# Optimization experiments

Hardware: AMD Instinct MI355X
Metric: run time of the kernel (lower is better)

## Reference

```python
import jax, jax.numpy as jnp
import numpy as np

B = 64      # batch
T = 32      # frames per clip
H = 256     # hidden_dim
NMAX = 64   # max boxes per batch element


def _n_per_frame():
    rng = np.random.default_rng(0)
    return rng.integers(32, NMAX + 1, size=B)  # each n <= NMAX


def setup_inputs() -> dict:
    n = _n_per_frame()
    N = int(n.sum())  # total boxes across batch (~3072)
    key = jax.random.key(0)
    k1, k2, k3 = jax.random.split(key, 3)
    bbox = jax.random.uniform(k1, (N * T, 4), dtype=jnp.float32)
    W1 = jax.random.normal(k2, (4, 128), dtype=jnp.float32) * 0.5
    b1 = jnp.zeros((128,), jnp.float32)
    W2 = jax.random.normal(k3, (128, H), dtype=jnp.float32) * 0.0884  # ~1/sqrt(128)
    b2 = jnp.zeros((H,), jnp.float32)
    return {
        "bbox": bbox,
        "W1": W1, "b1": b1, "W2": W2, "b2": b2,
        "n_per_frame": jnp.asarray(n, jnp.int32),
        "n_max": NMAX,
    }


def reference(bbox, W1, b1, W2, b2, n_per_frame, n_max):
    N = bbox.shape[0] // T  # static total box count
    # tiny MLP: 4 -> 128 -> H
    pos = (jax.nn.relu(bbox @ W1 + b1) @ W2 + b2).reshape(N, T, H)
    # ragged scatter into padded (B*n_max, T, H) tensor
    frame_id = jnp.repeat(jnp.arange(B), n_per_frame, total_repeat_length=N)  # [N]
    starts = jnp.cumsum(n_per_frame) - n_per_frame                            # exclusive cumsum [B]
    local = jnp.arange(N) - starts[frame_id]                                  # slot within frame
    tgt = frame_id * n_max + local                                            # [N] unique targets
    pos_pad = jnp.zeros((B * n_max, T, H), pos.dtype).at[tgt].set(pos)
    # (B, n_max, T, H) -> (B, T, n_max, H) -> (B*T, n_max, H) -> (n_max, B*T, H)
    out = (pos_pad.reshape(B, n_max, T, H)
           .transpose(0, 2, 1, 3)
           .reshape(B * T, n_max, H)
           .transpose(1, 0, 2))
    return out
```

## Files before the change

kernel.cpp:

```cpp
#include <hip/hip_runtime.h>

#define B_ 64
#define T_ 32
#define H_ 256
#define NMAX_ 64
#define TILES 2048
#define GRID 512
#define BLOCK 256

typedef __attribute__((ext_vector_type(8))) short short8;
typedef __attribute__((ext_vector_type(4))) float f32x4;

__device__ __forceinline__ short f2bf(float f) {
    unsigned u = __builtin_bit_cast(unsigned, f);
    u = (u + 0x7fffu + ((u >> 16) & 1u)) >> 16;
    return (short)u;
}

__global__ __launch_bounds__(BLOCK, 2)
void pe_fused(const float* __restrict__ bbox,
              const float* __restrict__ W1,
              const float* __restrict__ b1,
              const float* __restrict__ W2,
              const float* __restrict__ b2,
              const int*   __restrict__ npf,
              float* __restrict__ out,
              int NT)
{
    __shared__ float W1s[512];
    __shared__ float b1s[128];
    __shared__ int   s_n[64];
    __shared__ int   s_start[64];
    __shared__ short Hs[2][64 * 136];

    const int tid  = threadIdx.x;
    const int wave = tid >> 6;
    const int lane = tid & 63;
    const int q    = lane >> 4;
    const int m16  = lane & 15;

    if (tid < 256) { W1s[tid] = W1[tid]; W1s[tid + 256] = W1[tid + 256]; }
    if (tid < 128) b1s[tid] = b1[tid];

    if (wave == 0) {
        int v = npf[lane];
        s_n[lane] = v;
        int s = v;
#pragma unroll
        for (int d = 1; d < 64; d <<= 1) {
            int u = __shfl_up(s, d, 64);
            if (lane >= d) s += u;
        }
        s_start[lane] = s - v;
    }

    short8 Bf[4][4];
    float  b2v[4];
#pragma unroll
    for (int ct = 0; ct < 4; ++ct) {
        const int n = wave * 64 + ct * 16 + m16;
        b2v[ct] = b2[n];
#pragma unroll
        for (int kc = 0; kc < 4; ++kc) {
            const int k0 = kc * 32 + q * 8;
            short8 f;
#pragma unroll
            for (int jj = 0; jj < 8; ++jj)
                f[jj] = f2bf(W2[(k0 + jj) * H_ + n]);
            Bf[ct][kc] = f;
        }
    }
    __syncthreads();

    const int r4 = tid >> 2;
    const int c4 = tid & 3;

    int pbuf = 0;

    for (int tt = blockIdx.x; tt < TILES; tt += GRID) {
        const int b  = tt >> 5;
        const int l0 = (tt & 31) * 2;
        const int nb = s_n[b];

        const int ob0 = (l0 * (B_ * T_) + b * T_) * H_;
        const int ob1 = ob0 + (B_ * T_) * H_;

        if (l0 >= nb) {
            const float4 z = make_float4(0.f, 0.f, 0.f, 0.f);
#pragma unroll
            for (int rr = 0; rr < 16; ++rr) {
                const int r = rr * 4 + wave;
                float* dst = out + (r < 32 ? ob0 + r * H_ : ob1 + (r - 32) * H_);
                *(float4*)(dst + lane * 4) = z;
            }
            continue;
        }

        const int sb = s_start[b];

        {
            const int gr = (sb + l0) * T_ + r4;
            float4 bb = make_float4(0.f, 0.f, 0.f, 0.f);
            if (gr < NT) bb = *(const float4*)(bbox + gr * 4);
            short* hrow = &Hs[pbuf][r4 * 136 + c4 * 32];
#pragma unroll
            for (int w = 0; w < 4; ++w) {
                short8 hv;
#pragma unroll
                for (int jj = 0; jj < 8; ++jj) {
                    const int h = c4 * 32 + w * 8 + jj;
                    float v = b1s[h];
                    v = fmaf(bb.x, W1s[h],       v);
                    v = fmaf(bb.y, W1s[128 + h], v);
                    v = fmaf(bb.z, W1s[256 + h], v);
                    v = fmaf(bb.w, W1s[384 + h], v);
                    v = fmaxf(v, 0.f);
                    hv[jj] = f2bf(v);
                }
                *(short8*)(hrow + w * 8) = hv;
            }
        }
        __syncthreads();

        f32x4 acc[4][4];
#pragma unroll
        for (int rt = 0; rt < 4; ++rt)
#pragma unroll
            for (int ct = 0; ct < 4; ++ct)
                acc[rt][ct] = (f32x4){0.f, 0.f, 0.f, 0.f};

#pragma unroll
        for (int kc = 0; kc < 4; ++kc) {
            short8 a[4];
#pragma unroll
            for (int rt = 0; rt < 4; ++rt)
                a[rt] = *(const short8*)&Hs[pbuf][(rt * 16 + m16) * 136 + kc * 32 + q * 8];
#pragma unroll
            for (int rt = 0; rt < 4; ++rt)
#pragma unroll
                for (int ct = 0; ct < 4; ++ct)
                    acc[rt][ct] = __builtin_amdgcn_mfma_f32_16x16x32_bf16(
                        a[rt], Bf[ct][kc], acc[rt][ct], 0, 0, 0);
        }
        pbuf ^= 1;

        const bool v1 = (l0 + 1) < nb;
#pragma unroll
        for (int rt = 0; rt < 4; ++rt) {
#pragma unroll
            for (int reg = 0; reg < 4; ++reg) {
                const int rl = rt * 16 + q * 4 + reg;
                const bool ok = (rl < 32) | v1;
                float* dst = out + (rl < 32 ? ob0 + rl * H_ : ob1 + (rl - 32) * H_)
                                 + wave * 64 + m16;
#pragma unroll
                for (int ct = 0; ct < 4; ++ct)
                    dst[ct * 16] = ok ? (acc[rt][ct][reg] + b2v[ct]) : 0.f;
            }
        }
    }
}

extern "C" void kernel_launch(void* const* d_in, const int* in_sizes, int n_in,
                              void* d_out, int out_size, void* d_ws, size_t ws_size,
                              hipStream_t stream)
{
    const float* bbox = (const float*)d_in[0];
    const float* W1   = (const float*)d_in[1];
    const float* b1   = (const float*)d_in[2];
    const float* W2   = (const float*)d_in[3];
    const float* b2   = (const float*)d_in[4];
    const int*   npf  = (const int*)d_in[5];
    const int NT = in_sizes[0] / 4;

    pe_fused<<<GRID, BLOCK, 0, stream>>>(bbox, W1, b1, W2, b2, npf,
                                         (float*)d_out, NT);
}
```

Measured before the change: 157.2 us.

## Swap MFMA operands for float4 stores, prefetch bbox, use lighter barrier

Swaps the A/B operands of the MFMA so each lane's accumulator holds four consecutive output columns, which lets the epilogue write float4 vector stores instead of scalar stores. The bias b2 is loaded as float4 to match. All four tiles' bbox rows are prefetched into registers before the loop, and the loop is fully unrolled. __syncthreads is replaced by an inline-asm barrier that waits only on LDS counters, so outstanding global stores no longer block the barrier. This raises register pressure and relies on the fixed GRID*4 == TILES mapping.

```diff
diff --git a/kernel.cpp b/kernel.cpp
--- a/kernel.cpp
+++ b/kernel.cpp
@@ -15,6 +15,10 @@
     unsigned u = __builtin_bit_cast(unsigned, f);
     u = (u + 0x7fffu + ((u >> 16) & 1u)) >> 16;
     return (short)u;
+}
+
+__device__ __forceinline__ void barrier_nodrain() {
+    asm volatile("s_waitcnt lgkmcnt(0)\n\ts_barrier" ::: "memory");
 }
 
 __global__ __launch_bounds__(BLOCK, 2)
@@ -54,20 +58,19 @@
         s_start[lane] = s - v;
     }
 
-    short8 Bf[4][4];
-    float  b2v[4];
+    short8 Wf[4][4];
+    float4 b2q[4];
 #pragma unroll
     for (int ct = 0; ct < 4; ++ct) {
-        const int n = wave * 64 + ct * 16 + m16;
-        b2v[ct] = b2[n];
+        b2q[ct] = *(const float4*)(b2 + wave * 64 + ct * 16 + q * 4);
 #pragma unroll
         for (int kc = 0; kc < 4; ++kc) {
             const int k0 = kc * 32 + q * 8;
             short8 f;
 #pragma unroll
             for (int jj = 0; jj < 8; ++jj)
-                f[jj] = f2bf(W2[(k0 + jj) * H_ + n]);
-            Bf[ct][kc] = f;
+                f[jj] = f2bf(W2[(k0 + jj) * H_ + wave * 64 + ct * 16 + m16]);
+            Wf[ct][kc] = f;
         }
     }
     __syncthreads();
@@ -75,9 +78,22 @@
     const int r4 = tid >> 2;
     const int c4 = tid & 3;
 
+    float4 bb[4];
+#pragma unroll
+    for (int i = 0; i < 4; ++i) {
+        const int tt = blockIdx.x + i * GRID;
+        const int b  = tt >> 5;
+        const int l0 = (tt & 31) * 2;
+        const int g  = (s_start[b] + l0) * T_ + r4;
+        bb[i] = make_float4(0.f, 0.f, 0.f, 0.f);
+        if (g < NT) bb[i] = *(const float4*)(bbox + g * 4);
+    }
+
     int pbuf = 0;
 
-    for (int tt = blockIdx.x; tt < TILES; tt += GRID) {
+#pragma unroll
+    for (int i = 0; i < 4; ++i) {
+        const int tt = blockIdx.x + i * GRID;
         const int b  = tt >> 5;
         const int l0 = (tt & 31) * 2;
         const int nb = s_n[b];
@@ -96,12 +112,8 @@
             continue;
         }
 
-        const int sb = s_start[b];
-
         {
-            const int gr = (sb + l0) * T_ + r4;
-            float4 bb = make_float4(0.f, 0.f, 0.f, 0.f);
-            if (gr < NT) bb = *(const float4*)(bbox + gr * 4);
+            const float4 bv = bb[i];
             short* hrow = &Hs[pbuf][r4 * 136 + c4 * 32];
 #pragma unroll
             for (int w = 0; w < 4; ++w) {
@@ -110,52 +122,54 @@
                 for (int jj = 0; jj < 8; ++jj) {
                     const int h = c4 * 32 + w * 8 + jj;
                     float v = b1s[h];
-                    v = fmaf(bb.x, W1s[h],       v);
-                    v = fmaf(bb.y, W1s[128 + h], v);
-                    v = fmaf(bb.z, W1s[256 + h], v);
-                    v = fmaf(bb.w, W1s[384 + h], v);
+                    v = fmaf(bv.x, W1s[h],       v);
+                    v = fmaf(bv.y, W1s[128 + h], v);
+                    v = fmaf(bv.z, W1s[256 + h], v);
+                    v = fmaf(bv.w, W1s[384 + h], v);
                     v = fmaxf(v, 0.f);
                     hv[jj] = f2bf(v);
                 }
                 *(short8*)(hrow + w * 8) = hv;
             }
         }
-        __syncthreads();
+        barrier_nodrain();
 
         f32x4 acc[4][4];
 #pragma unroll
-        for (int rt = 0; rt < 4; ++rt)
+        for (int ct = 0; ct < 4; ++ct)
 #pragma unroll
-            for (int ct = 0; ct < 4; ++ct)
-                acc[rt][ct] = (f32x4){0.f, 0.f, 0.f, 0.f};
+            for (int rt = 0; rt < 4; ++rt)
+                acc[ct][rt] = (f32x4){0.f, 0.f, 0.f, 0.f};
 
 #pragma unroll
         for (int kc = 0; kc < 4; ++kc) {
-            short8 a[4];
+            short8 hf[4];
 #pragma unroll
             for (int rt = 0; rt < 4; ++rt)
-                a[rt] = *(const short8*)&Hs[pbuf][(rt * 16 + m16) * 136 + kc * 32 + q * 8];
+                hf[rt] = *(const short8*)&Hs[pbuf][(rt * 16 + m16) * 136 + kc * 32 + q * 8];
 #pragma unroll
-            for (int rt = 0; rt < 4; ++rt)
+            for (int ct = 0; ct < 4; ++ct)
 #pragma unroll
-                for (int ct = 0; ct < 4; ++ct)
-                    acc[rt][ct] = __builtin_amdgcn_mfma_f32_16x16x32_bf16(
-                        a[rt], Bf[ct][kc], acc[rt][ct], 0, 0, 0);
+                for (int rt = 0; rt < 4; ++rt)
+                    acc[ct][rt] = __builtin_amdgcn_mfma_f32_16x16x32_bf16(
+                        Wf[ct][kc], hf[rt], acc[ct][rt], 0, 0, 0);
         }
         pbuf ^= 1;
 
         const bool v1 = (l0 + 1) < nb;
 #pragma unroll
         for (int rt = 0; rt < 4; ++rt) {
+            const int rl = rt * 16 + m16;
+            const bool ok = (rt < 2) | v1;
+            float* base = out + (rt < 2 ? ob0 + rl * H_ : ob1 + (rl - 32) * H_)
+                              + wave * 64 + q * 4;
 #pragma unroll
-            for (int reg = 0; reg < 4; ++reg) {
-                const int rl = rt * 16 + q * 4 + reg;
-                const bool ok = (rl < 32) | v1;
-                float* dst = out + (rl < 32 ? ob0 + rl * H_ : ob1 + (rl - 32) * H_)
-                                 + wave * 64 + m16;
-#pragma unroll
-                for (int ct = 0; ct < 4; ++ct)
-                    dst[ct * 16] = ok ? (acc[rt][ct][reg] + b2v[ct]) : 0.f;
+            for (int ct = 0; ct < 4; ++ct) {
+                const f32x4 d = acc[ct][rt];
+                float4 v = make_float4(0.f, 0.f, 0.f, 0.f);
+                if (ok) v = make_float4(d[0] + b2q[ct].x, d[1] + b2q[ct].y,
+                                        d[2] + b2q[ct].z, d[3] + b2q[ct].w);
+                *(float4*)(base + ct * 16) = v;
             }
         }
     }
```

Result: faster. 153.2 us (-2.5%).
